# Performance work log

Hardware: AMD Instinct MI355X
Metric: run time of the kernel (lower is better)

## Reference

```python
import jax, jax.numpy as jnp
import numpy as np

B, C, G, K, SC = 4, 128, 64, 3, 512  # batch, per-branch channels (h_in=l_in), groups, kernel, style channels
EPS = 1e-5
H = 256  # hf spatial; lf spatial = H//2


def rpad(x, p):
    return jnp.pad(x, ((0, 0), (0, 0), (p, p), (p, p)), mode='reflect')


def conv(x, w, groups=1):
    return jax.lax.conv_general_dilated(
        x, w, (1, 1), 'VALID',
        dimension_numbers=('NCHW', 'OIHW', 'NCHW'),
        feature_group_count=groups)


def inorm(x):
    # F.instance_norm / InstanceNorm2d (affine=False, eps=1e-5)
    m = x.mean((2, 3), keepdims=True)
    v = x.var((2, 3), keepdims=True)
    return (x - m) * jax.lax.rsqrt(v + EPS)


def lrelu(x):
    return jnp.where(x >= 0, x, 0.2 * x)


def predict(s, sp_w, sp_b, pw_w, pw_b, b_w, b_b):
    # spatial kernel predictor: reflect-pad + conv, output spatial is exactly KxK
    sp = conv(rpad(s, (K - 1) // 2), sp_w) + sp_b[None, :, None, None]  # [B, C*C/G, K, K]
    w_spatial = sp.reshape(s.shape[0], C, C // G, K, K)
    sm = s.mean((2, 3))  # AdaptiveAvgPool2d((1,1)) -> [B, SC]
    w_pointwise = (sm @ pw_w.T + pw_b).reshape(s.shape[0], C, C // G, 1, 1)
    bias = sm @ b_w.T + b_b  # [B, C]
    return w_spatial, w_pointwise, bias


def ada_conv(x, w_sp, w_pw, bias, cw, cb):
    x = inorm(x)
    p = (K - 1) // 2

    def single(xi, ws, wp, bi):
        y = conv(rpad(xi[None], p), ws, groups=G)             # grouped spatial conv
        y = conv(y, wp, groups=G) + bi[None, :, None, None]   # grouped pointwise conv + bias
        return y[0]

    y = jax.vmap(single)(x, w_sp, w_pw, bias)
    y = conv(rpad(y, 1), cw) + cb[None, :, None, None]        # shared 3x3 conv (reflect pad)
    return y


def setup_inputs() -> dict:
    key = jax.random.key(0)
    ks = jax.random.split(key, 20)
    s = 0.05
    inp = {
        'c_hf': jax.random.normal(ks[0], (B, C, H, H), jnp.float32),
        'c_lf': jax.random.normal(ks[1], (B, C, H // 2, H // 2), jnp.float32),
        's_hf': jax.random.normal(ks[2], (B, SC, K, K), jnp.float32),
        's_lf': jax.random.normal(ks[3], (B, SC, K, K), jnp.float32),
        # KernelPredictor (high branch)
        'kp_h_sp_w': jax.random.normal(ks[4], (C * C // G, SC, K, K), jnp.float32) * s,
        'kp_h_sp_b': jax.random.normal(ks[5], (C * C // G,), jnp.float32) * s,
        'kp_h_pw_w': jax.random.normal(ks[6], (C * C // G, SC), jnp.float32) * s,
        'kp_h_pw_b': jax.random.normal(ks[7], (C * C // G,), jnp.float32) * s,
        'kp_h_b_w': jax.random.normal(ks[8], (C, SC), jnp.float32) * s,
        'kp_h_b_b': jax.random.normal(ks[9], (C,), jnp.float32) * s,
        # KernelPredictor (low branch)
        'kp_l_sp_w': jax.random.normal(ks[10], (C * C // G, SC, K, K), jnp.float32) * s,
        'kp_l_sp_b': jax.random.normal(ks[11], (C * C // G,), jnp.float32) * s,
        'kp_l_pw_w': jax.random.normal(ks[12], (C * C // G, SC), jnp.float32) * s,
        'kp_l_pw_b': jax.random.normal(ks[13], (C * C // G,), jnp.float32) * s,
        'kp_l_b_w': jax.random.normal(ks[14], (C, SC), jnp.float32) * s,
        'kp_l_b_b': jax.random.normal(ks[15], (C,), jnp.float32) * s,
        # shared convs inside AdaConv2d
        'conv_h_w': jax.random.normal(ks[16], (C, C, 3, 3), jnp.float32) * s,
        'conv_h_b': jax.random.normal(ks[17], (C,), jnp.float32) * s,
        'conv_l_w': jax.random.normal(ks[18], (C, C, 3, 3), jnp.float32) * s,
        'conv_l_b': jax.random.normal(ks[19], (C,), jnp.float32) * s,
    }
    return inp


def reference(c_hf, c_lf, s_hf, s_lf,
              kp_h_sp_w, kp_h_sp_b, kp_h_pw_w, kp_h_pw_b, kp_h_b_w, kp_h_b_b,
              kp_l_sp_w, kp_l_sp_b, kp_l_pw_w, kp_l_pw_b, kp_l_b_w, kp_l_b_b,
              conv_h_w, conv_h_b, conv_l_w, conv_l_b):
    h_ws, h_wp, h_b = predict(s_hf, kp_h_sp_w, kp_h_sp_b, kp_h_pw_w, kp_h_pw_b, kp_h_b_w, kp_h_b_b)
    l_ws, l_wp, l_b = predict(s_lf, kp_l_sp_w, kp_l_sp_b, kp_l_pw_w, kp_l_pw_b, kp_l_b_w, kp_l_b_b)
    oh = ada_conv(c_hf, h_ws, h_wp, h_b, conv_h_w, conv_h_b)
    ol = ada_conv(c_lf, l_ws, l_wp, l_b, conv_l_w, conv_l_b)
    # Oct_conv_norm ('in') + Oct_conv_lreLU(0.2)
    oh = lrelu(inorm(oh))
    ol = lrelu(inorm(ol))
    return (oh, ol)
```

## Files before the change

kernel.cpp:

```cpp
#include <hip/hip_runtime.h>
#include <hip/hip_bf16.h>

#define BB 4
#define CCH 128
#define GRP 64
#define SCH 512
#define EPSV 1e-5f

typedef unsigned short u16;

__device__ __forceinline__ float b2f(u16 u) {
    return __uint_as_float(((unsigned int)u) << 16);
}
__device__ __forceinline__ u16 f2b(float f) {
    unsigned int u = __float_as_uint(f);
    return (u16)((u + 0x7fffu + ((u >> 16) & 1u)) >> 16);
}
__device__ __forceinline__ int refl(int i, int n) {
    if (i < 0) i = -i;
    if (i >= n) i = 2 * n - 2 - i;
    return i;
}
__device__ __forceinline__ float ldv(const void* p, long long i, int isbf) {
    return isbf ? b2f(((const u16*)p)[i]) : ((const float*)p)[i];
}
__device__ __forceinline__ void stv(void* p, long long i, int isbf, float v) {
    if (isbf) ((u16*)p)[i] = f2b(v);
    else ((float*)p)[i] = v;
}

__global__ __launch_bounds__(256) void detect_kernel(const void* x, int* flag) {
    const u16* p = (const u16*)x;
    int tid = threadIdx.x;
    int cnt = 0;
#pragma unroll
    for (int k = 0; k < 16; ++k) {
        float v = fabsf(b2f(p[2 * (tid * 16 + k)]));
        if (v > 0.004f && v < 8.0f) cnt++;
    }
    __shared__ int red[256];
    red[tid] = cnt;
    __syncthreads();
    for (int st = 128; st > 0; st >>= 1) {
        if (tid < st) red[tid] += red[tid + st];
        __syncthreads();
    }
    if (tid == 0) flag[0] = (red[0] >= 2048) ? 1 : 0;
}

__global__ __launch_bounds__(256) void sm_kernel(const int* flag, const void* s, float* sm) {
    int idx = blockIdx.x * 256 + threadIdx.x;
    if (idx >= BB * SCH) return;
    int isbf = flag[0];
    float t = 0.f;
#pragma unroll
    for (int j = 0; j < 9; ++j) t += ldv(s, (long long)idx * 9 + j, isbf);
    sm[idx] = t * (1.0f / 9.0f);
}

__global__ __launch_bounds__(256) void spconv_kernel(const int* flag, const void* s,
                                                     const void* sp_w, const void* sp_b,
                                                     float* wsp_out) {
    int isbf = flag[0];
    int b = blockIdx.x >> 8;
    int oc = blockIdx.x & 255;
    int tid = threadIdx.x;
    float acc[9];
#pragma unroll
    for (int o = 0; o < 9; ++o) acc[o] = 0.f;
    for (int ic = tid; ic < SCH; ic += 256) {
        float sv[9], wv[9];
#pragma unroll
        for (int j = 0; j < 9; ++j) sv[j] = ldv(s, (long long)(b * SCH + ic) * 9 + j, isbf);
#pragma unroll
        for (int j = 0; j < 9; ++j) wv[j] = ldv(sp_w, (long long)(oc * SCH + ic) * 9 + j, isbf);
        const int m[5] = {1, 0, 1, 2, 1};
#pragma unroll
        for (int oy = 0; oy < 3; ++oy) {
#pragma unroll
            for (int ox = 0; ox < 3; ++ox) {
                float t = 0.f;
#pragma unroll
                for (int kr = 0; kr < 3; ++kr)
#pragma unroll
                    for (int kc = 0; kc < 3; ++kc)
                        t += sv[m[oy + kr] * 3 + m[ox + kc]] * wv[kr * 3 + kc];
                acc[oy * 3 + ox] += t;
            }
        }
    }
    __shared__ float red[256];
#pragma unroll 1
    for (int o = 0; o < 9; ++o) {
        red[tid] = acc[o];
        __syncthreads();
        for (int st = 128; st > 0; st >>= 1) {
            if (tid < st) red[tid] += red[tid + st];
            __syncthreads();
        }
        if (tid == 0) wsp_out[(b * 256 + oc) * 9 + o] = red[0] + ldv(sp_b, oc, isbf);
        __syncthreads();
    }
}

__global__ __launch_bounds__(256) void pwbias_kernel(const int* flag, const float* __restrict__ sm,
                                                     const void* pw_w, const void* pw_b,
                                                     const void* b_w, const void* b_b,
                                                     float* wpw, float* biasout) {
    int idx = blockIdx.x * 256 + threadIdx.x;
    if (idx >= BB * 384) return;
    int isbf = flag[0];
    int b = idx / 384;
    int j = idx % 384;
    const float* smb = sm + b * SCH;
    if (j < 256) {
        float a = 0.f;
        for (int k = 0; k < SCH; ++k) a += smb[k] * ldv(pw_w, (long long)j * SCH + k, isbf);
        wpw[b * 256 + j] = a + ldv(pw_b, j, isbf);
    } else {
        int j2 = j - 256;
        float a = 0.f;
        for (int k = 0; k < SCH; ++k) a += smb[k] * ldv(b_w, (long long)j2 * SCH + k, isbf);
        biasout[b * CCH + j2] = a + ldv(b_b, j2, isbf);
    }
}

__global__ __launch_bounds__(256) void stats_kernel(const int* flag, const void* x, long long off,
                                                    float* stat, int HW) {
    int isbf = flag[0];
    int bc = blockIdx.x;
    int tid = threadIdx.x;
    long long base = off + (long long)bc * HW;
    float s = 0.f, s2 = 0.f;
    for (int i = tid; i < HW; i += 256) {
        float v = ldv(x, base + i, isbf);
        s += v;
        s2 += v * v;
    }
    __shared__ float rs[256];
    __shared__ float rq[256];
    rs[tid] = s;
    rq[tid] = s2;
    __syncthreads();
    for (int st = 128; st > 0; st >>= 1) {
        if (tid < st) { rs[tid] += rs[tid + st]; rq[tid] += rq[tid + st]; }
        __syncthreads();
    }
    if (tid == 0) {
        float inv = 1.0f / (float)HW;
        float mean = rs[0] * inv;
        float var = rq[0] * inv - mean * mean;
        stat[bc * 2] = mean;
        stat[bc * 2 + 1] = rsqrtf(var + EPSV);
    }
}

__global__ __launch_bounds__(256) void grouped_band_kernel(const int* flag, const void* x,
                                                           const float* __restrict__ xstat,
                                                           const float* __restrict__ wsp,
                                                           const float* __restrict__ wpw,
                                                           const float* __restrict__ bias,
                                                           float* __restrict__ band,
                                                           int H, int W, int r0) {
    int isbf = flag[0];
    int ppb = (34 * W) >> 8;
    int t = blockIdx.x;
    int bg = t / ppb;
    int tile = t - bg * ppb;
    int b = bg >> 6;
    int g = bg & 63;
    int tid = threadIdx.x;

    __shared__ float sw[36], pw[4], bs[2], xm[2], xr[2];
    if (tid < 36) {
        int o = tid / 18, i = (tid % 18) / 9, k = tid % 9;
        sw[tid] = wsp[(b * 256 + (2 * g + o) * 2 + i) * 9 + k];
    }
    if (tid < 4) pw[tid] = wpw[b * 256 + (2 * g + (tid >> 1)) * 2 + (tid & 1)];
    if (tid < 2) {
        bs[tid] = bias[b * CCH + 2 * g + tid];
        xm[tid] = xstat[(b * CCH + 2 * g + tid) * 2];
        xr[tid] = xstat[(b * CCH + 2 * g + tid) * 2 + 1];
    }
    __syncthreads();

    int p = tile * 256 + tid;
    int j = p / W;
    int col = p - j * W;
    int grow = refl(r0 - 1 + j, H);

    float y10 = 0.f, y11 = 0.f;
#pragma unroll
    for (int i = 0; i < 2; ++i) {
        long long xb = (long long)(b * CCH + 2 * g + i) * H * W;
        float m = xm[i], r = xr[i];
#pragma unroll
        for (int kr = 0; kr < 3; ++kr) {
            int rr = refl(grow + kr - 1, H) * W;
#pragma unroll
            for (int kc = 0; kc < 3; ++kc) {
                int cc = refl(col + kc - 1, W);
                float xv = (ldv(x, xb + rr + cc, isbf) - m) * r;
                y10 += xv * sw[i * 9 + kr * 3 + kc];
                y11 += xv * sw[18 + i * 9 + kr * 3 + kc];
            }
        }
    }
    band[((long long)(b * CCH + 2 * g) * 34 + j) * W + col] = pw[0] * y10 + pw[1] * y11 + bs[0];
    band[((long long)(b * CCH + 2 * g + 1) * 34 + j) * W + col] = pw[2] * y10 + pw[3] * y11 + bs[1];
}

__global__ __launch_bounds__(256, 2) void bigconv_tile_kernel(
    const int* flag, const float* __restrict__ band,
    const void* cw, const void* cb, void* out, long long ooff,
    int H, int W, int r0, int nbands, long long bandstride) {
    int isbf = flag[0];
    int ctiles = W >> 6;
    int per_band = BB * 32 * ctiles;
    int t = blockIdx.x;
    int bandidx = t / per_band;
    int rem = t - bandidx * per_band;
    int b = rem / (32 * ctiles);
    int rem2 = rem - b * (32 * ctiles);
    int ocb = rem2 / ctiles;
    int tx0 = (rem2 - ocb * ctiles) << 6;
    int rr0 = r0 + 32 * bandidx;
    const float* bandb = band + bandidx * bandstride + (long long)b * CCH * 34 * W;

    int tid = threadIdx.x;
    int tr = tid >> 4;
    int tc = tid & 15;

    __shared__ float wsh[4608];
    __shared__ float ins[9248];

    for (int idx = tid; idx < 4608; idx += 256) {
        int ic = idx / 36;
        int r = idx - ic * 36;
        int ol = r / 9;
        int k = r - ol * 9;
        wsh[idx] = ldv(cw, ((long long)(ocb * 4 + ol) * CCH + ic) * 9 + k, isbf);
    }

    float acc[32];
#pragma unroll
    for (int ol = 0; ol < 4; ++ol) {
        float bv = ldv(cb, ocb * 4 + ol, isbf);
#pragma unroll
        for (int p = 0; p < 8; ++p) acc[ol * 8 + p] = bv;
    }

    int gcl = refl(tx0 - 1, W);
    int gcr = refl(tx0 + 64, W);

#pragma unroll 1
    for (int icc = 0; icc < 32; ++icc) {
        float4 bodyv[9];
        float hv[2];
#pragma unroll
        for (int k = 0; k < 9; ++k) {
            int rowid = k * 16 + tr;
            if (rowid < 136) {
                bodyv[k] = *reinterpret_cast<const float4*>(
                    bandb + (long long)(icc * 136 + rowid) * W + tx0 + tc * 4);
            }
        }
#pragma unroll
        for (int k = 0; k < 2; ++k) {
            int h = k * 256 + tid;
            if (h < 272) {
                int rh = h >> 1;
                int side = h & 1;
                hv[k] = bandb[(long long)(icc * 136 + rh) * W + (side ? gcr : gcl)];
            }
        }
        __syncthreads();
#pragma unroll
        for (int k = 0; k < 9; ++k) {
            int rowid = k * 16 + tr;
            if (rowid < 136) {
                int icl = rowid / 34;
                int rr = rowid - icl * 34;
                float* d = &ins[icl * 2312 + rr * 68 + 1 + tc * 4];
                d[0] = bodyv[k].x; d[1] = bodyv[k].y; d[2] = bodyv[k].z; d[3] = bodyv[k].w;
            }
        }
#pragma unroll
        for (int k = 0; k < 2; ++k) {
            int h = k * 256 + tid;
            if (h < 272) {
                int rh = h >> 1;
                int side = h & 1;
                int icl = rh / 34;
                int rr = rh - icl * 34;
                ins[icl * 2312 + rr * 68 + (side ? 65 : 0)] = hv[k];
            }
        }
        __syncthreads();

#pragma unroll
        for (int icl = 0; icl < 4; ++icl) {
            float wr[36];
            const float* wp = &wsh[(icc * 4 + icl) * 36];
#pragma unroll
            for (int k = 0; k < 9; ++k) {
                float4 w4 = *reinterpret_cast<const float4*>(wp + 4 * k);
                wr[4 * k] = w4.x; wr[4 * k + 1] = w4.y;
                wr[4 * k + 2] = w4.z; wr[4 * k + 3] = w4.w;
            }
            float win[32];
            const float* ip = &ins[icl * 2312 + (tr * 2) * 68 + tc * 4];
#pragma unroll
            for (int jj = 0; jj < 4; ++jj) {
                float4 lo = *reinterpret_cast<const float4*>(ip + jj * 68);
                float4 hi = *reinterpret_cast<const float4*>(ip + jj * 68 + 4);
                win[jj * 8 + 0] = lo.x; win[jj * 8 + 1] = lo.y;
                win[jj * 8 + 2] = lo.z; win[jj * 8 + 3] = lo.w;
                win[jj * 8 + 4] = hi.x; win[jj * 8 + 5] = hi.y;
                win[jj * 8 + 6] = hi.z; win[jj * 8 + 7] = hi.w;
            }
#pragma unroll
            for (int ol = 0; ol < 4; ++ol)
#pragma unroll
                for (int py = 0; py < 2; ++py)
#pragma unroll
                    for (int px = 0; px < 4; ++px) {
                        float a = acc[ol * 8 + py * 4 + px];
#pragma unroll
                        for (int kr = 0; kr < 3; ++kr)
#pragma unroll
                            for (int kc = 0; kc < 3; ++kc)
                                a += win[(py + kr) * 8 + px + kc] * wr[ol * 9 + kr * 3 + kc];
                        acc[ol * 8 + py * 4 + px] = a;
                    }
        }
    }

#pragma unroll
    for (int ol = 0; ol < 4; ++ol) {
        long long oco = ooff + (long long)(b * CCH + ocb * 4 + ol) * H * W;
#pragma unroll
        for (int py = 0; py < 2; ++py) {
            long long rowo = oco + (long long)(rr0 + tr * 2 + py) * W + tx0 + tc * 4;
#pragma unroll
            for (int px = 0; px < 4; ++px)
                stv(out, rowo + px, isbf, acc[ol * 8 + py * 4 + px]);
        }
    }
}

__global__ __launch_bounds__(256) void finalize_kernel(const int* flag, void* y, long long off,
                                                       const float* __restrict__ stat,
                                                       int HW, long long total) {
    long long idx = (long long)blockIdx.x * 256 + threadIdx.x;
    if (idx >= total) return;
    int isbf = flag[0];
    int bc = (int)(idx / HW);
    float m = stat[bc * 2];
    float r = stat[bc * 2 + 1];
    float v = (ldv(y, off + idx, isbf) - m) * r;
    stv(y, off + idx, isbf, v >= 0.f ? v : 0.2f * v);
}

extern "C" void kernel_launch(void* const* d_in, const int* in_sizes, int n_in,
                              void* d_out, int out_size, void* d_ws, size_t ws_size,
                              hipStream_t stream) {
    const void* c_hf = d_in[0];
    const void* c_lf = d_in[1];
    const void* s_hf = d_in[2];
    const void* s_lf = d_in[3];
    const void* kp_h_sp_w = d_in[4];
    const void* kp_h_sp_b = d_in[5];
    const void* kp_h_pw_w = d_in[6];
    const void* kp_h_pw_b = d_in[7];
    const void* kp_h_b_w = d_in[8];
    const void* kp_h_b_b = d_in[9];
    const void* kp_l_sp_w = d_in[10];
    const void* kp_l_sp_b = d_in[11];
    const void* kp_l_pw_w = d_in[12];
    const void* kp_l_pw_b = d_in[13];
    const void* kp_l_b_w = d_in[14];
    const void* kp_l_b_b = d_in[15];
    const void* conv_h_w = d_in[16];
    const void* conv_h_b = d_in[17];
    const void* conv_l_w = d_in[18];
    const void* conv_l_b = d_in[19];

    int* flag = (int*)d_ws;
    float* f = (float*)d_ws;
    float* sm_h = f + 64;
    float* sm_l = f + 2112;
    float* wsp_h = f + 4160;
    float* wsp_l = f + 13376;
    float* wpw_h = f + 22592;
    float* wpw_l = f + 23616;
    float* bias_h = f + 24640;
    float* bias_l = f + 25152;
    float* xstat_h = f + 25664;
    float* xstat_l = f + 26688;
    float* ystat_h = f + 27712;
    float* ystat_l = f + 28736;
    float* band = (float*)((char*)d_ws + 131072);

    const int HWH = 256 * 256, HWL = 128 * 128;
    const long long OFF_L = 33554432LL;
    const long long BSTR_L = 4LL * 128 * 34 * 128;

    detect_kernel<<<1, 256, 0, stream>>>(c_hf, flag);

    sm_kernel<<<8, 256, 0, stream>>>(flag, s_hf, sm_h);
    sm_kernel<<<8, 256, 0, stream>>>(flag, s_lf, sm_l);
    spconv_kernel<<<1024, 256, 0, stream>>>(flag, s_hf, kp_h_sp_w, kp_h_sp_b, wsp_h);
    spconv_kernel<<<1024, 256, 0, stream>>>(flag, s_lf, kp_l_sp_w, kp_l_sp_b, wsp_l);
    pwbias_kernel<<<6, 256, 0, stream>>>(flag, sm_h, kp_h_pw_w, kp_h_pw_b, kp_h_b_w, kp_h_b_b, wpw_h, bias_h);
    pwbias_kernel<<<6, 256, 0, stream>>>(flag, sm_l, kp_l_pw_w, kp_l_pw_b, kp_l_b_w, kp_l_b_b, wpw_l, bias_l);

    stats_kernel<<<512, 256, 0, stream>>>(flag, c_hf, 0, xstat_h, HWH);
    stats_kernel<<<512, 256, 0, stream>>>(flag, c_lf, 0, xstat_l, HWL);

    for (int r0 = 0; r0 < 256; r0 += 32) {
        grouped_band_kernel<<<4 * 64 * 34, 256, 0, stream>>>(flag, c_hf, xstat_h, wsp_h, wpw_h,
                                                             bias_h, band, 256, 256, r0);
        bigconv_tile_kernel<<<512, 256, 0, stream>>>(flag, band, conv_h_w, conv_h_b,
                                                     d_out, 0, 256, 256, r0, 1, 0);
    }
    for (int r0 = 0; r0 < 128; r0 += 64) {
        grouped_band_kernel<<<4 * 64 * 17, 256, 0, stream>>>(flag, c_lf, xstat_l, wsp_l, wpw_l,
                                                             bias_l, band, 128, 128, r0);
        grouped_band_kernel<<<4 * 64 * 17, 256, 0, stream>>>(flag, c_lf, xstat_l, wsp_l, wpw_l,
                                                             bias_l, band + BSTR_L, 128, 128, r0 + 32);
        bigconv_tile_kernel<<<512, 256, 0, stream>>>(flag, band, conv_l_w, conv_l_b,
                                                     d_out, OFF_L, 128, 128, r0, 2, BSTR_L);
    }

    stats_kernel<<<512, 256, 0, stream>>>(flag, d_out, 0, ystat_h, HWH);
    stats_kernel<<<512, 256, 0, stream>>>(flag, d_out, OFF_L, ystat_l, HWL);
    finalize_kernel<<<131072, 256, 0, stream>>>(flag, d_out, 0, ystat_h, HWH, (long long)BB * CCH * HWH);
    finalize_kernel<<<32768, 256, 0, stream>>>(flag, d_out, OFF_L, ystat_l, HWL, (long long)BB * CCH * HWL);
}
```

Before: 2.618 ms.

## Pre-pad band buffer and double-buffer global loads in 3x3 conv tile

```diff
diff --git a/kernel.cpp b/kernel.cpp
--- a/kernel.cpp
+++ b/kernel.cpp
@@ -161,9 +161,10 @@
                                                            const float* __restrict__ wpw,
                                                            const float* __restrict__ bias,
                                                            float* __restrict__ band,
-                                                           int H, int W, int r0) {
-    int isbf = flag[0];
-    int ppb = (34 * W) >> 8;
+                                                           int H, int W, int WS, int r0) {
+    int isbf = flag[0];
+    int WP = W + 2;
+    int ppb = (34 * WP + 255) >> 8;
     int t = blockIdx.x;
     int bg = t / ppb;
     int tile = t - bg * ppb;
@@ -185,8 +186,10 @@
     __syncthreads();
 
     int p = tile * 256 + tid;
-    int j = p / W;
-    int col = p - j * W;
+    int j = p / WP;
+    int colp = p - j * WP;
+    if (j >= 34) return;
+    int ct = refl(colp - 1, W);
     int grow = refl(r0 - 1 + j, H);
 
     float y10 = 0.f, y11 = 0.f;
@@ -199,21 +202,21 @@
             int rr = refl(grow + kr - 1, H) * W;
 #pragma unroll
             for (int kc = 0; kc < 3; ++kc) {
-                int cc = refl(col + kc - 1, W);
+                int cc = refl(ct + kc - 1, W);
                 float xv = (ldv(x, xb + rr + cc, isbf) - m) * r;
                 y10 += xv * sw[i * 9 + kr * 3 + kc];
                 y11 += xv * sw[18 + i * 9 + kr * 3 + kc];
             }
         }
     }
-    band[((long long)(b * CCH + 2 * g) * 34 + j) * W + col] = pw[0] * y10 + pw[1] * y11 + bs[0];
-    band[((long long)(b * CCH + 2 * g + 1) * 34 + j) * W + col] = pw[2] * y10 + pw[3] * y11 + bs[1];
+    band[((long long)(b * CCH + 2 * g) * 34 + j) * WS + colp] = pw[0] * y10 + pw[1] * y11 + bs[0];
+    band[((long long)(b * CCH + 2 * g + 1) * 34 + j) * WS + colp] = pw[2] * y10 + pw[3] * y11 + bs[1];
 }
 
 __global__ __launch_bounds__(256, 2) void bigconv_tile_kernel(
     const int* flag, const float* __restrict__ band,
     const void* cw, const void* cb, void* out, long long ooff,
-    int H, int W, int r0, int nbands, long long bandstride) {
+    int H, int W, int WS, int r0, long long bandstride) {
     int isbf = flag[0];
     int ctiles = W >> 6;
     int per_band = BB * 32 * ctiles;
@@ -225,7 +228,7 @@
     int ocb = rem2 / ctiles;
     int tx0 = (rem2 - ocb * ctiles) << 6;
     int rr0 = r0 + 32 * bandidx;
-    const float* bandb = band + bandidx * bandstride + (long long)b * CCH * 34 * W;
+    const float* bandb = band + bandidx * bandstride + (long long)b * CCH * 34 * WS;
 
     int tid = threadIdx.x;
     int tr = tid >> 4;
@@ -250,91 +253,93 @@
         for (int p = 0; p < 8; ++p) acc[ol * 8 + p] = bv;
     }
 
-    int gcl = refl(tx0 - 1, W);
-    int gcr = refl(tx0 + 64, W);
+    int lwoff[9];
+#pragma unroll
+    for (int k = 0; k < 9; ++k) {
+        int rowid = k * 16 + tr;
+        int icl = rowid / 34;
+        int rr = rowid - icl * 34;
+        lwoff[k] = icl * 2312 + rr * 68 + tc * 4;
+    }
+    const float* gbase = bandb + tx0 + tc * 4;
+    int rh0 = tid >> 1, sd0 = tid & 1;
+    int i0 = rh0 / 34;
+    int lh0 = i0 * 2312 + (rh0 - i0 * 34) * 68 + 64 + sd0;
+    long long gh0 = (long long)rh0 * WS + tx0 + 64 + sd0;
+    int rh1 = 128 + (tid >> 1), sd1 = tid & 1;
+    int i1 = rh1 / 34;
+    int lh1 = i1 * 2312 + (rh1 - i1 * 34) * 68 + 64 + sd1;
+    long long gh1 = (long long)rh1 * WS + tx0 + 64 + sd1;
+    long long cstep = 136LL * WS;
+
+#define BC_LOADS(BV, HV, ICC)                                                        \
+    {                                                                                \
+        const float* pc_ = gbase + (long long)(ICC) * cstep;                         \
+        _Pragma("unroll") for (int k = 0; k < 9; ++k) {                              \
+            if (k < 8 || tr < 8)                                                     \
+                BV[k] = *reinterpret_cast<const float4*>(pc_ + (k * 16 + tr) * WS);  \
+        }                                                                            \
+        HV[0] = bandb[(long long)(ICC) * cstep + gh0];                               \
+        if (tid < 16) HV[1] = bandb[(long long)(ICC) * cstep + gh1];                 \
+    }
+
+#define BC_WRITES(BV, HV)                                                            \
+    {                                                                                \
+        _Pragma("unroll") for (int k = 0; k < 9; ++k) {                              \
+            if (k < 8 || tr < 8) *reinterpret_cast<float4*>(&ins[lwoff[k]]) = BV[k]; \
+        }                                                                            \
+        ins[lh0] = HV[0];                                                            \
+        if (tid < 16) ins[lh1] = HV[1];                                              \
+    }
+
+#define BC_COMPUTE(ICC)                                                              \
+    _Pragma("unroll") for (int icl = 0; icl < 4; ++icl) {                            \
+        float win[32];                                                               \
+        const float* ip_ = &ins[icl * 2312 + (tr * 2) * 68 + tc * 4];                \
+        _Pragma("unroll") for (int jj = 0; jj < 4; ++jj) {                           \
+            float4 lo = *reinterpret_cast<const float4*>(ip_ + jj * 68);             \
+            float4 hi = *reinterpret_cast<const float4*>(ip_ + jj * 68 + 4);         \
+            win[jj * 8 + 0] = lo.x; win[jj * 8 + 1] = lo.y;                          \
+            win[jj * 8 + 2] = lo.z; win[jj * 8 + 3] = lo.w;                          \
+            win[jj * 8 + 4] = hi.x; win[jj * 8 + 5] = hi.y;                          \
+            win[jj * 8 + 6] = hi.z; win[jj * 8 + 7] = hi.w;                          \
+        }                                                                            \
+        const float* wp_ = &wsh[((ICC) * 4 + icl) * 36];                             \
+        _Pragma("unroll") for (int ol = 0; ol < 4; ++ol) {                           \
+            float wr[9];                                                             \
+            _Pragma("unroll") for (int k = 0; k < 9; ++k) wr[k] = wp_[ol * 9 + k];   \
+            _Pragma("unroll") for (int py = 0; py < 2; ++py)                         \
+                _Pragma("unroll") for (int px = 0; px < 4; ++px) {                   \
+                    float a = acc[ol * 8 + py * 4 + px];                             \
+                    _Pragma("unroll") for (int kr = 0; kr < 3; ++kr)                 \
+                        _Pragma("unroll") for (int kc = 0; kc < 3; ++kc)             \
+                            a += win[(py + kr) * 8 + px + kc] * wr[kr * 3 + kc];     \
+                    acc[ol * 8 + py * 4 + px] = a;                                   \
+                }                                                                    \
+        }                                                                            \
+    }
+
+    float4 bvA[9], bvB[9];
+    float hA[2], hB[2];
+    BC_LOADS(bvA, hA, 0);
 
 #pragma unroll 1
-    for (int icc = 0; icc < 32; ++icc) {
-        float4 bodyv[9];
-        float hv[2];
-#pragma unroll
-        for (int k = 0; k < 9; ++k) {
-            int rowid = k * 16 + tr;
-            if (rowid < 136) {
-                bodyv[k] = *reinterpret_cast<const float4*>(
-                    bandb + (long long)(icc * 136 + rowid) * W + tx0 + tc * 4);
-            }
-        }
-#pragma unroll
-        for (int k = 0; k < 2; ++k) {
-            int h = k * 256 + tid;
-            if (h < 272) {
-                int rh = h >> 1;
-                int side = h & 1;
-                hv[k] = bandb[(long long)(icc * 136 + rh) * W + (side ? gcr : gcl)];
-            }
-        }
-        __syncthreads();
-#pragma unroll
-        for (int k = 0; k < 9; ++k) {
-            int rowid = k * 16 + tr;
-            if (rowid < 136) {
-                int icl = rowid / 34;
-                int rr = rowid - icl * 34;
-                float* d = &ins[icl * 2312 + rr * 68 + 1 + tc * 4];
-                d[0] = bodyv[k].x; d[1] = bodyv[k].y; d[2] = bodyv[k].z; d[3] = bodyv[k].w;
-            }
-        }
-#pragma unroll
-        for (int k = 0; k < 2; ++k) {
-            int h = k * 256 + tid;
-            if (h < 272) {
-                int rh = h >> 1;
-                int side = h & 1;
-                int icl = rh / 34;
-                int rr = rh - icl * 34;
-                ins[icl * 2312 + rr * 68 + (side ? 65 : 0)] = hv[k];
-            }
-        }
-        __syncthreads();
-
-#pragma unroll
-        for (int icl = 0; icl < 4; ++icl) {
-            float wr[36];
-            const float* wp = &wsh[(icc * 4 + icl) * 36];
-#pragma unroll
-            for (int k = 0; k < 9; ++k) {
-                float4 w4 = *reinterpret_cast<const float4*>(wp + 4 * k);
-                wr[4 * k] = w4.x; wr[4 * k + 1] = w4.y;
-                wr[4 * k + 2] = w4.z; wr[4 * k + 3] = w4.w;
-            }
-            float win[32];
-            const float* ip = &ins[icl * 2312 + (tr * 2) * 68 + tc * 4];
-#pragma unroll
-            for (int jj = 0; jj < 4; ++jj) {
-                float4 lo = *reinterpret_cast<const float4*>(ip + jj * 68);
-                float4 hi = *reinterpret_cast<const float4*>(ip + jj * 68 + 4);
-                win[jj * 8 + 0] = lo.x; win[jj * 8 + 1] = lo.y;
-                win[jj * 8 + 2] = lo.z; win[jj * 8 + 3] = lo.w;
-                win[jj * 8 + 4] = hi.x; win[jj * 8 + 5] = hi.y;
-                win[jj * 8 + 6] = hi.z; win[jj * 8 + 7] = hi.w;
-            }
-#pragma unroll
-            for (int ol = 0; ol < 4; ++ol)
-#pragma unroll
-                for (int py = 0; py < 2; ++py)
-#pragma unroll
-                    for (int px = 0; px < 4; ++px) {
-                        float a = acc[ol * 8 + py * 4 + px];
-#pragma unroll
-                        for (int kr = 0; kr < 3; ++kr)
-#pragma unroll
-                            for (int kc = 0; kc < 3; ++kc)
-                                a += win[(py + kr) * 8 + px + kc] * wr[ol * 9 + kr * 3 + kc];
-                        acc[ol * 8 + py * 4 + px] = a;
-                    }
-        }
-    }
+    for (int ii = 0; ii < 16; ++ii) {
+        int icc0 = ii * 2;
+        __syncthreads();
+        BC_WRITES(bvA, hA);
+        __syncthreads();
+        BC_LOADS(bvB, hB, icc0 + 1);
+        BC_COMPUTE(icc0);
+        __syncthreads();
+        BC_WRITES(bvB, hB);
+        __syncthreads();
+        if (ii < 15) BC_LOADS(bvA, hA, icc0 + 2);
+        BC_COMPUTE(icc0 + 1);
+    }
+#undef BC_LOADS
+#undef BC_WRITES
+#undef BC_COMPUTE
 
 #pragma unroll
     for (int ol = 0; ol < 4; ++ol) {
@@ -403,8 +408,9 @@
     float* band = (float*)((char*)d_ws + 131072);
 
     const int HWH = 256 * 256, HWL = 128 * 128;
+    const int WSH = 256 + 8, WSL = 128 + 8;
     const long long OFF_L = 33554432LL;
-    const long long BSTR_L = 4LL * 128 * 34 * 128;
+    const long long BSTR_L = 4LL * 128 * 34 * WSL;
 
     detect_kernel<<<1, 256, 0, stream>>>(c_hf, flag);
 
@@ -418,19 +424,22 @@
     stats_kernel<<<512, 256, 0, stream>>>(flag, c_hf, 0, xstat_h, HWH);
     stats_kernel<<<512, 256, 0, stream>>>(flag, c_lf, 0, xstat_l, HWL);
 
+    const int GB_H = 256 * ((34 * (256 + 2) + 255) >> 8);
+    const int GB_L = 256 * ((34 * (128 + 2) + 255) >> 8);
+
     for (int r0 = 0; r0 < 256; r0 += 32) {
-        grouped_band_kernel<<<4 * 64 * 34, 256, 0, stream>>>(flag, c_hf, xstat_h, wsp_h, wpw_h,
-                                                             bias_h, band, 256, 256, r0);
+        grouped_band_kernel<<<GB_H, 256, 0, stream>>>(flag, c_hf, xstat_h, wsp_h, wpw_h,
+                                                      bias_h, band, 256, 256, WSH, r0);
         bigconv_tile_kernel<<<512, 256, 0, stream>>>(flag, band, conv_h_w, conv_h_b,
-                                                     d_out, 0, 256, 256, r0, 1, 0);
+                                                     d_out, 0, 256, 256, WSH, r0, 0);
     }
     for (int r0 = 0; r0 < 128; r0 += 64) {
-        grouped_band_kernel<<<4 * 64 * 17, 256, 0, stream>>>(flag, c_lf, xstat_l, wsp_l, wpw_l,
-                                                             bias_l, band, 128, 128, r0);
-        grouped_band_kernel<<<4 * 64 * 17, 256, 0, stream>>>(flag, c_lf, xstat_l, wsp_l, wpw_l,
-                                                             bias_l, band + BSTR_L, 128, 128, r0 + 32);
+        grouped_band_kernel<<<GB_L, 256, 0, stream>>>(flag, c_lf, xstat_l, wsp_l, wpw_l,
+                                                      bias_l, band, 128, 128, WSL, r0);
+        grouped_band_kernel<<<GB_L, 256, 0, stream>>>(flag, c_lf, xstat_l, wsp_l, wpw_l,
+                                                      bias_l, band + BSTR_L, 128, 128, WSL, r0 + 32);
         bigconv_tile_kernel<<<512, 256, 0, stream>>>(flag, band, conv_l_w, conv_l_b,
-                                                     d_out, OFF_L, 128, 128, r0, 2, BSTR_L);
+                                                     d_out, OFF_L, 128, 128, WSL, r0, BSTR_L);
     }
 
     stats_kernel<<<512, 256, 0, stream>>>(flag, d_out, 0, ystat_h, HWH);
```

Result: slower. 5.733 ms (+119.0%).
